# Kernel tuning notes

Measured on AMD Instinct MI355X. Metric: run time of the kernel, lower is better.

Reference implementation:

```python
import jax, jax.numpy as jnp
import numpy as np

B, T = 64, 512
OBS, DM, DS, NL = 115, 128, 8, 3
EMB, NA, H1 = 16, 19, 256


def _ln(x, g, b, eps=1e-5):
    m = jnp.mean(x, -1, keepdims=True)
    v = jnp.mean((x - m) ** 2, -1, keepdims=True)
    return (x - m) * jax.lax.rsqrt(v + eps) * g + b


def _s6(x, h, lng, lnb, w_ig, w_dt, b_dt, a_log, w_b, w_c, d_par, w_out):
    # x: [B,T,DM], h: [B,DM,DS]
    xn = _ln(x, lng, lnb)
    xp = xn @ w_ig.T                               # [B,T,2*DM]
    x_in, z = xp[..., :DM], xp[..., DM:]
    dt = jax.nn.softplus(x_in @ w_dt.T + b_dt)     # [B,T,DM]
    A = -jnp.exp(a_log)                            # [DM,DS]
    bt = x_in @ w_b.T                              # [B,T,DS]
    ct = x_in @ w_c.T                              # [B,T,DS]
    dA = jnp.exp(dt[..., None] * A)                # [B,T,DM,DS]
    upd = (dt * x_in)[..., None] * bt[:, :, None, :]  # [B,T,DM,DS]

    def step(hc, inp):
        dA_t, u_t, c_t = inp
        hn = dA_t * hc + u_t                       # [B,DM,DS]
        y = jnp.einsum('bds,bs->bd', hn, c_t)      # [B,DM]
        return hn, y

    h_f, ys = jax.lax.scan(
        step, h,
        (jnp.swapaxes(dA, 0, 1), jnp.swapaxes(upd, 0, 1), jnp.swapaxes(ct, 0, 1)))
    y = jnp.swapaxes(ys, 0, 1)                     # [B,T,DM]
    ssm = y * jax.nn.silu(z) + x_in * d_par
    return x + ssm @ w_out.T, h_f.reshape(h_f.shape[0], -1)


def _forward(prev_actions, obs, h0, enc_w1, enc_b1, enc_g1, enc_bb1, enc_w2, enc_b2,
             enc_g2, enc_bb2, emb, proj_w, proj_b, proj_g, proj_bb,
             m_ln_g, m_ln_b, m_w_ig, m_w_dt, m_b_dt, m_a_log, m_w_b, m_w_c, m_d, m_w_out,
             fn_g, fn_b, pol_w1, pol_b1, pol_g, pol_bb, pol_w2, pol_b2):
    # MLP encoder: Linear -> LN -> SiLU -> Linear -> LN (final norm)
    e = jax.nn.silu(_ln(obs @ enc_w1.T + enc_b1, enc_g1, enc_bb1))
    e = _ln(e @ enc_w2.T + enc_b2, enc_g2, enc_bb2)
    pa = emb[prev_actions]                         # [B,T,EMB]
    x = jnp.concatenate([e, pa], -1) @ proj_w.T + proj_b
    x = jax.nn.silu(_ln(x, proj_g, proj_bb))
    for i in range(NL):
        x, _ = _s6(x, h0[i].reshape(-1, DM, DS), m_ln_g[i], m_ln_b[i], m_w_ig[i],
                   m_w_dt[i], m_b_dt[i], m_a_log[i], m_w_b[i], m_w_c[i], m_d[i], m_w_out[i])
    x = _ln(x, fn_g, fn_b)
    p = jax.nn.silu(_ln(x @ pol_w1.T + pol_b1, pol_g, pol_bb))
    return p @ pol_w2.T + pol_b2                   # [B,T,NA] policy logits


def setup_inputs() -> dict:
    key = jax.random.key(0)
    ks = iter(jax.random.split(key, 64))
    def n(shape, s=0.05):
        return jax.random.normal(next(ks), shape, dtype=jnp.float32) * s
    return {
        'obs': jax.random.normal(next(ks), (B, T, OBS), dtype=jnp.float32),
        'h0': jnp.zeros((NL, B, DM * DS), jnp.float32),
        'enc_w1': n((H1, OBS)), 'enc_b1': jnp.zeros((H1,)),
        'enc_g1': jnp.ones((H1,)), 'enc_bb1': jnp.zeros((H1,)),
        'enc_w2': n((DM, H1)), 'enc_b2': jnp.zeros((DM,)),
        'enc_g2': jnp.ones((DM,)), 'enc_bb2': jnp.zeros((DM,)),
        'emb': n((NA + 1, EMB), 1.0),
        'proj_w': n((DM, DM + EMB)), 'proj_b': jnp.zeros((DM,)),
        'proj_g': jnp.ones((DM,)), 'proj_bb': jnp.zeros((DM,)),
        'm_ln_g': jnp.ones((NL, DM)), 'm_ln_b': jnp.zeros((NL, DM)),
        'm_w_ig': n((NL, 2 * DM, DM)), 'm_w_dt': n((NL, DM, DM)),
        'm_b_dt': jnp.zeros((NL, DM)),
        'm_a_log': jax.random.uniform(next(ks), (NL, DM, DS), minval=-3.0, maxval=-1.0, dtype=jnp.float32),
        'm_w_b': n((NL, DS, DM)), 'm_w_c': n((NL, DS, DM)),
        'm_d': jnp.ones((NL, DM)), 'm_w_out': n((NL, DM, DM)),
        'fn_g': jnp.ones((DM,)), 'fn_b': jnp.zeros((DM,)),
        'pol_w1': n((DM, DM)), 'pol_b1': jnp.zeros((DM,)),
        'pol_g': jnp.ones((DM,)), 'pol_bb': jnp.zeros((DM,)),
        'pol_w2': n((NA, DM)), 'pol_b2': jnp.zeros((NA,)),
        'prev_actions': jax.random.randint(next(ks), (B, T), 0, NA + 1),
    }


def reference(obs, h0, enc_w1, enc_b1, enc_g1, enc_bb1, enc_w2, enc_b2, enc_g2, enc_bb2,
              emb, proj_w, proj_b, proj_g, proj_bb, m_ln_g, m_ln_b, m_w_ig, m_w_dt,
              m_b_dt, m_a_log, m_w_b, m_w_c, m_d, m_w_out, fn_g, fn_b, pol_w1, pol_b1,
              pol_g, pol_bb, pol_w2, pol_b2, prev_actions):
    return _forward(prev_actions, obs, h0, enc_w1, enc_b1, enc_g1, enc_bb1, enc_w2,
                    enc_b2, enc_g2, enc_bb2, emb, proj_w, proj_b, proj_g, proj_bb,
                    m_ln_g, m_ln_b, m_w_ig, m_w_dt, m_b_dt, m_a_log, m_w_b, m_w_c,
                    m_d, m_w_out, fn_g, fn_b, pol_w1, pol_b1, pol_g, pol_bb, pol_w2, pol_b2)
```

## Files before the change

kernel.cpp:

```cpp
#include <hip/hip_runtime.h>
#include <math.h>

#define BB 64
#define TT 512
#define OBSD 115
#define DMD 128
#define DSD 8
#define NLD 3
#define EMBD 16
#define NAD 19
#define H1D 256
#define NTOK (BB*TT)
#define SSEG 32
#define TSEG (TT/SSEG)

typedef unsigned short ushort_t;
typedef __attribute__((ext_vector_type(8))) short short8;
typedef __attribute__((ext_vector_type(4))) float f32x4;

__device__ __forceinline__ float silu_f(float x){ return x / (1.f + __expf(-x)); }
__device__ __forceinline__ float softplus_f(float x){
  return fmaxf(x, 0.f) + log1pf(__expf(-fabsf(x)));
}
__device__ __forceinline__ ushort_t f2bf(float x){
  unsigned u = __float_as_uint(x);
  unsigned r = (u + 0x7fffu + ((u >> 16) & 1u)) >> 16;
  return (ushort_t)r;
}
__device__ __forceinline__ float b2f(ushort_t x){
  return __uint_as_float(((unsigned)x) << 16);
}
#define MFMA(a,b,c) __builtin_amdgcn_mfma_f32_16x16x32_bf16((a),(b),(c),0,0,0)
#define LOG2E 1.44269504f

struct PJob { const float* src; ushort_t* dst; int N; int K; int Kpad; int rowofs; int Nw; };
struct PJobs { PJob j[20]; };

__global__ __launch_bounds__(256) void k_prep(PJobs P){
  const int job = blockIdx.x >> 2;
  const int sub = blockIdx.x & 3;
  PJob pj = P.j[job];
  const int elems = pj.Nw * pj.Kpad;
  for (int idx = sub*256 + threadIdx.x; idx < elems; idx += 4*256){
    int n = idx / pj.Kpad;
    int k = idx - n*pj.Kpad;
    float v = (n < pj.N && k < pj.K) ? pj.src[(size_t)n*pj.K + k] : 0.f;
    pj.dst[(size_t)(pj.rowofs + n)*pj.Kpad + k] = f2bf(v);
  }
}

__global__ __launch_bounds__(256, 8) void k_enc12p(
    const float* __restrict__ obs, const ushort_t* __restrict__ w1b,
    const float* __restrict__ b1, const float* __restrict__ g1,
    const float* __restrict__ bb1,
    const ushort_t* __restrict__ w2b,
    const float* __restrict__ b2, const float* __restrict__ g2,
    const float* __restrict__ bb2,
    const float* __restrict__ emb, const int* __restrict__ pact,
    const ushort_t* __restrict__ pwb, const float* __restrict__ pb,
    const float* __restrict__ pg, const float* __restrict__ pbb,
    float* __restrict__ X,
    const float* __restrict__ lng, const float* __restrict__ lnb,
    const ushort_t* __restrict__ wigb, const ushort_t* __restrict__ wdbcb,
    const float* __restrict__ bdt,
    ushort_t* __restrict__ XINb, ushort_t* __restrict__ Zb,
    ushort_t* __restrict__ DTb, ushort_t* __restrict__ BTu, ushort_t* __restrict__ CTu,
    const float* __restrict__ alog0,
    float* __restrict__ HLOC, float* __restrict__ PPR)
{
  __shared__ __align__(16) char sm[15104];
  ushort_t* s_obs = (ushort_t*)sm;
  ushort_t* s_e1  = (ushort_t*)sm;
  ushort_t* s_xin = (ushort_t*)sm;
  ushort_t* s_dt  = (ushort_t*)(sm + 4352);
  ushort_t* s_a2  = (ushort_t*)(sm + 8448);
  ushort_t* s_btc = (ushort_t*)(sm + 13824);
  float2*   s_st  = (float2*)(sm + 14080);
  float2*   s_st2 = (float2*)(sm + 14592);

  const int tok0 = blockIdx.x * 16;
  const int bidx = blockIdx.x >> 5;
  const int ch   = blockIdx.x & 31;
  const int tid = threadIdx.x;
  const int lane = tid & 63, w = tid >> 6;
  const int q = lane >> 4, cn = lane & 15;

  {
    const int t = tid >> 4, kc = tid & 15;
    const float* op = obs + (size_t)(tok0 + t)*OBSD;
    short8 v;
    #pragma unroll
    for (int j = 0; j < 8; j++){
      int k = kc*8 + j;
      v[j] = (short)f2bf(k < OBSD ? op[k] : 0.f);
    }
    *(short8*)&s_obs[t*136 + kc*8] = v;
  }
  for (int e = tid; e < 16*32; e += 256){
    int t = e >> 5, k = e & 31;
    float v = 0.f;
    if (k < EMBD){ int a = pact[tok0 + t]; v = emb[(size_t)a*EMBD + k]; }
    s_a2[t*168 + 128 + k] = f2bf(v);
  }
  __syncthreads();

  f32x4 acc[4];
  {
    short8 af[4];
    #pragma unroll
    for (int ks = 0; ks < 4; ks++)
      af[ks] = *(const short8*)&s_obs[cn*136 + ks*32 + q*8];
    #pragma unroll
    for (int nt = 0; nt < 4; nt++){
      const int n0 = (w*4 + nt) * 16;
      f32x4 a = {0.f,0.f,0.f,0.f};
      #pragma unroll
      for (int ks = 0; ks < 4; ks++){
        short8 bf = *(const short8*)&w1b[(size_t)(n0 + cn)*128 + ks*32 + q*8];
        a = MFMA(af[ks], bf, a);
      }
      float bv = b1[n0 + cn];
      #pragma unroll
      for (int r = 0; r < 4; r++) a[r] += bv;
      acc[nt] = a;
    }
    #pragma unroll
    for (int r = 0; r < 4; r++){
      float s = 0.f, s2 = 0.f;
      #pragma unroll
      for (int nt = 0; nt < 4; nt++){ float v = acc[nt][r]; s += v; s2 = fmaf(v, v, s2); }
      s += __shfl_xor(s, 1, 64); s2 += __shfl_xor(s2, 1, 64);
      s += __shfl_xor(s, 2, 64); s2 += __shfl_xor(s2, 2, 64);
      s += __shfl_xor(s, 4, 64); s2 += __shfl_xor(s2, 4, 64);
      s += __shfl_xor(s, 8, 64); s2 += __shfl_xor(s2, 8, 64);
      if (cn == 0) s_st[(q*4 + r)*4 + w] = make_float2(s, s2);
    }
  }
  __syncthreads();

  {
    float mu[4], rs[4];
    #pragma unroll
    for (int r = 0; r < 4; r++){
      const int row = q*4 + r;
      float2 p0 = s_st[row*4+0], p1 = s_st[row*4+1];
      float2 p2 = s_st[row*4+2], p3 = s_st[row*4+3];
      float s = p0.x+p1.x+p2.x+p3.x, s2 = p0.y+p1.y+p2.y+p3.y;
      float m = s * (1.f/256.f);
      mu[r] = m;
      rs[r] = rsqrtf(s2 * (1.f/256.f) - m*m + 1e-5f);
    }
    #pragma unroll
    for (int nt = 0; nt < 4; nt++){
      const int col = (w*4 + nt)*16 + cn;
      float gg = g1[col], bbv = bb1[col];
      #pragma unroll
      for (int r = 0; r < 4; r++){
        float v = (acc[nt][r] - mu[r]) * rs[r] * gg + bbv;
        s_e1[(q*4 + r)*264 + col] = f2bf(silu_f(v));
      }
    }
  }
  __syncthreads();

  f32x4 acc2[2];
  {
    short8 af2[8];
    #pragma unroll
    for (int ks = 0; ks < 8; ks++)
      af2[ks] = *(const short8*)&s_e1[cn*264 + ks*32 + q*8];
    #pragma unroll
    for (int nt = 0; nt < 2; nt++){
      const int n0 = (w*2 + nt) * 16;
      f32x4 a = {0.f,0.f,0.f,0.f};
      #pragma unroll
      for (int ks = 0; ks < 8; ks++){
        short8 bf = *(const short8*)&w2b[(size_t)(n0 + cn)*256 + ks*32 + q*8];
        a = MFMA(af2[ks], bf, a);
      }
      float bv = b2[n0 + cn];
      #pragma unroll
      for (int r = 0; r < 4; r++) a[r] += bv;
      acc2[nt] = a;
    }
    #pragma unroll
    for (int r = 0; r < 4; r++){
      float s = 0.f, s2 = 0.f;
      #pragma unroll
      for (int nt = 0; nt < 2; nt++){ float v = acc2[nt][r]; s += v; s2 = fmaf(v, v, s2); }
      s += __shfl_xor(s, 1, 64); s2 += __shfl_xor(s2, 1, 64);
      s += __shfl_xor(s, 2, 64); s2 += __shfl_xor(s2, 2, 64);
      s += __shfl_xor(s, 4, 64); s2 += __shfl_xor(s2, 4, 64);
      s += __shfl_xor(s, 8, 64); s2 += __shfl_xor(s2, 8, 64);
      if (cn == 0) s_st[(q*4 + r)*4 + w] = make_float2(s, s2);
    }
  }
  __syncthreads();

  {
    float mu[4], rs[4];
    #pragma unroll
    for (int r = 0; r < 4; r++){
      const int row = q*4 + r;
      float2 p0 = s_st[row*4+0], p1 = s_st[row*4+1];
      float2 p2 = s_st[row*4+2], p3 = s_st[row*4+3];
      float s = p0.x+p1.x+p2.x+p3.x, s2 = p0.y+p1.y+p2.y+p3.y;
      float m = s * (1.f/128.f);
      mu[r] = m;
      rs[r] = rsqrtf(s2 * (1.f/128.f) - m*m + 1e-5f);
    }
    #pragma unroll
    for (int nt = 0; nt < 2; nt++){
      const int col = (w*2 + nt)*16 + cn;
      float gg = g2[col], bbv = bb2[col];
      #pragma unroll
      for (int r = 0; r < 4; r++){
        float v = (acc2[nt][r] - mu[r]) * rs[r] * gg + bbv;
        s_a2[(q*4 + r)*168 + col] = f2bf(v);
      }
    }
  }
  __syncthreads();

  f32x4 acc3[2];
  {
    short8 af3[5];
    #pragma unroll
    for (int ks = 0; ks < 5; ks++)
      af3[ks] = *(const short8*)&s_a2[cn*168 + ks*32 + q*8];
    #pragma unroll
    for (int nt = 0; nt < 2; nt++){
      const int n0 = (w*2 + nt) * 16;
      f32x4 a = {0.f,0.f,0.f,0.f};
      #pragma unroll
      for (int ks = 0; ks < 5; ks++){
        short8 bf = *(const short8*)&pwb[(size_t)(n0 + cn)*160 + ks*32 + q*8];
        a = MFMA(af3[ks], bf, a);
      }
      float bv = pb[n0 + cn];
      #pragma unroll
      for (int r = 0; r < 4; r++) a[r] += bv;
      acc3[nt] = a;
    }
    #pragma unroll
    for (int r = 0; r < 4; r++){
      float s = 0.f, s2 = 0.f;
      #pragma unroll
      for (int nt = 0; nt < 2; nt++){ float v = acc3[nt][r]; s += v; s2 = fmaf(v, v, s2); }
      s += __shfl_xor(s, 1, 64); s2 += __shfl_xor(s2, 1, 64);
      s += __shfl_xor(s, 2, 64); s2 += __shfl_xor(s2, 2, 64);
      s += __shfl_xor(s, 4, 64); s2 += __shfl_xor(s2, 4, 64);
      s += __shfl_xor(s, 8, 64); s2 += __shfl_xor(s2, 8, 64);
      if (cn == 0) s_st[(q*4 + r)*4 + w] = make_float2(s, s2);
    }
  }
  __syncthreads();

  {
    float mu[4], rs[4];
    #pragma unroll
    for (int r = 0; r < 4; r++){
      const int row = q*4 + r;
      float2 p0 = s_st[row*4+0], p1 = s_st[row*4+1];
      float2 p2 = s_st[row*4+2], p3 = s_st[row*4+3];
      float s = p0.x+p1.x+p2.x+p3.x, s2 = p0.y+p1.y+p2.y+p3.y;
      float m = s * (1.f/128.f);
      mu[r] = m;
      rs[r] = rsqrtf(s2 * (1.f/128.f) - m*m + 1e-5f);
    }
    float ps[4] = {0.f,0.f,0.f,0.f}, ps2[4] = {0.f,0.f,0.f,0.f};
    #pragma unroll
    for (int nt = 0; nt < 2; nt++){
      const int col = (w*2 + nt)*16 + cn;
      float gg = pg[col], bbv = pbb[col];
      #pragma unroll
      for (int r = 0; r < 4; r++){
        float v = (acc3[nt][r] - mu[r]) * rs[r] * gg + bbv;
        v = silu_f(v);
        acc3[nt][r] = v;
        X[(size_t)(tok0 + q*4 + r)*128 + col] = v;
        ps[r] += v; ps2[r] = fmaf(v, v, ps2[r]);
      }
    }
    #pragma unroll
    for (int r = 0; r < 4; r++){
      float s = ps[r], s2 = ps2[r];
      s += __shfl_xor(s, 1, 64); s2 += __shfl_xor(s2, 1, 64);
      s += __shfl_xor(s, 2, 64); s2 += __shfl_xor(s2, 2, 64);
      s += __shfl_xor(s, 4, 64); s2 += __shfl_xor(s2, 4, 64);
      s += __shfl_xor(s, 8, 64); s2 += __shfl_xor(s2, 8, 64);
      if (cn == 0) s_st2[(q*4 + r)*4 + w] = make_float2(s, s2);
    }
  }
  __syncthreads();

  {
    float mu[4], rs[4];
    #pragma unroll
    for (int r = 0; r < 4; r++){
      const int row = q*4 + r;
      float2 p0 = s_st2[row*4+0], p1 = s_st2[row*4+1];
      float2 p2 = s_st2[row*4+2], p3 = s_st2[row*4+3];
      float s = p0.x+p1.x+p2.x+p3.x, s2 = p0.y+p1.y+p2.y+p3.y;
      float m = s * (1.f/128.f);
      mu[r] = m;
      rs[r] = rsqrtf(s2 * (1.f/128.f) - m*m + 1e-5f);
    }
    #pragma unroll
    for (int nt = 0; nt < 2; nt++){
      const int col = (w*2 + nt)*16 + cn;
      float gg = lng[col], bbv = lnb[col];
      #pragma unroll
      for (int r = 0; r < 4; r++){
        float v = (acc3[nt][r] - mu[r]) * rs[r] * gg + bbv;
        s_a2[(q*4 + r)*168 + col] = f2bf(v);
      }
    }
  }
  __syncthreads();

  {
    short8 af[4];
    #pragma unroll
    for (int ks = 0; ks < 4; ks++)
      af[ks] = *(const short8*)&s_a2[cn*168 + ks*32 + q*8];
    #pragma unroll
    for (int i = 0; i < 4; i++){
      const int n0 = (w*4 + i) * 16;
      f32x4 a = {0.f,0.f,0.f,0.f};
      #pragma unroll
      for (int ks = 0; ks < 4; ks++){
        short8 bf = *(const short8*)&wigb[(size_t)(n0 + cn)*128 + ks*32 + q*8];
        a = MFMA(af[ks], bf, a);
      }
      if (n0 < 128){
        #pragma unroll
        for (int r = 0; r < 4; r++){
          int tr = q*4 + r;
          ushort_t bb = f2bf(a[r]);
          XINb[(size_t)(tok0 + tr)*128 + n0 + cn] = bb;
          s_xin[tr*136 + n0 + cn] = bb;
        }
      } else {
        #pragma unroll
        for (int r = 0; r < 4; r++){
          int tr = q*4 + r;
          Zb[(size_t)(tok0 + tr)*128 + (n0 - 128) + cn] = f2bf(a[r]);
        }
      }
    }
  }
  __syncthreads();

  {
    short8 af2[4];
    #pragma unroll
    for (int ks = 0; ks < 4; ks++)
      af2[ks] = *(const short8*)&s_xin[cn*136 + ks*32 + q*8];
    for (int nt = w; nt < 9; nt += 4){
      const int n0 = nt * 16;
      f32x4 a = {0.f,0.f,0.f,0.f};
      #pragma unroll
      for (int ks = 0; ks < 4; ks++){
        short8 bf = *(const short8*)&wdbcb[(size_t)(n0 + cn)*128 + ks*32 + q*8];
        a = MFMA(af2[ks], bf, a);
      }
      const int col = n0 + cn;
      if (col < 128){
        float bd = bdt[col];
        #pragma unroll
        for (int r = 0; r < 4; r++){
          int tr = q*4 + r;
          ushort_t dv = f2bf(softplus_f(a[r] + bd));
          DTb[(size_t)(tok0 + tr)*128 + col] = dv;
          s_dt[tr*136 + col] = dv;
        }
      } else if (col < 136){
        #pragma unroll
        for (int r = 0; r < 4; r++){
          int tr = q*4 + r;
          ushort_t bb = f2bf(a[r]);
          BTu[(size_t)(tok0 + tr)*8 + (col - 128)] = bb;
          s_btc[tr*8 + (col - 128)] = bb;
        }
      } else {
        #pragma unroll
        for (int r = 0; r < 4; r++)
          CTu[(size_t)(tok0 + q*4 + r)*8 + (col - 136)] = f2bf(a[r]);
      }
    }
  }
  __syncthreads();

  {
    const int d = tid & 127, sh = tid >> 7;
    float A2c[4], hh[4], pp[4];
    #pragma unroll
    for (int j = 0; j < 4; j++){
      A2c[j] = -__expf(alog0[d*8 + sh*4 + j]) * LOG2E;
      hh[j] = 0.f; pp[j] = 1.f;
    }
    #pragma unroll 4
    for (int t = 0; t < 16; t++){
      float dt = b2f(s_dt[t*136 + d]);
      float wv = dt * b2f(s_xin[t*136 + d]);
      #pragma unroll
      for (int j = 0; j < 4; j++){
        float dA = exp2f(dt * A2c[j]);
        hh[j] = fmaf(dA, hh[j], wv * b2f(s_btc[t*8 + sh*4 + j]));
        pp[j] *= dA;
      }
    }
    const size_t o = ((size_t)bidx*SSEG + ch)*1024 + d*8 + sh*4;
    #pragma unroll
    for (int j = 0; j < 4; j++){ HLOC[o+j] = hh[j]; PPR[o+j] = pp[j]; }
  }
}

__global__ __launch_bounds__(256) void k_carry(
    float* __restrict__ HL, const float* __restrict__ PP,
    const float* __restrict__ h0g)
{
  const int idx = blockIdx.x*256 + threadIdx.x;
  const size_t base = (size_t)(idx >> 10) * (SSEG*1024) + (idx & 1023);
  float hl[SSEG], pp[SSEG];
  #pragma unroll
  for (int ch = 0; ch < SSEG; ch++){
    hl[ch] = HL[base + (size_t)ch*1024];
    pp[ch] = PP[base + (size_t)ch*1024];
  }
  float h = h0g[idx];
  #pragma unroll
  for (int ch = 0; ch < SSEG; ch++){
    HL[base + (size_t)ch*1024] = h;
    h = fmaf(pp[ch], h, hl[ch]);
  }
}

#define SMB 17664

__device__ __forceinline__ void phaseB16(
    const ushort_t* DTb, const ushort_t* XINb, const ushort_t* Zb,
    const ushort_t* BTu, const ushort_t* CTu,
    const float* __restrict__ alog, const float* __restrict__ HLpre,
    const float* __restrict__ dpar, const ushort_t* __restrict__ woutb,
    float* __restrict__ X, char* sm, int b, int seg, int tid)
{
  ushort_t* s_dtS = (ushort_t*)sm;
  ushort_t* s_xiS = (ushort_t*)(sm + 4096);
  ushort_t* s_zS  = (ushort_t*)(sm + 8192);
  float*    s_x   = (float*)sm;
  ushort_t* s_a   = (ushort_t*)(sm + 12288);
  ushort_t* s_bt  = (ushort_t*)(sm + 16640);
  ushort_t* s_ct  = (ushort_t*)(sm + 16896);
  float2*   s_st  = (float2*)(sm + 17152);

  const int lane = tid & 63, w = tid >> 6, q = lane >> 4, cn = lane & 15;
  const size_t segtok = (size_t)b*TT + seg*TSEG;

  float xpre[2][4];
  #pragma unroll
  for (int i = 0; i < 2; i++){
    const int n0 = (w*2 + i) * 16;
    #pragma unroll
    for (int r = 0; r < 4; r++)
      xpre[i][r] = X[(segtok + q*4 + r)*128 + n0 + cn];
  }

  ((uint4*)s_dtS)[tid] = ((const uint4*)(DTb  + segtok*128))[tid];
  ((uint4*)s_xiS)[tid] = ((const uint4*)(XINb + segtok*128))[tid];
  ((uint4*)s_zS )[tid] = ((const uint4*)(Zb   + segtok*128))[tid];
  if (tid < 64){
    ((unsigned*)s_bt)[tid] = ((const unsigned*)(BTu + segtok*8))[tid];
    ((unsigned*)s_ct)[tid] = ((const unsigned*)(CTu + segtok*8))[tid];
  }

  const int d2 = (w << 5) | (lane & 31);
  const int sh = lane >> 5;
  float A2h[4], h[4];
  {
    const size_t o = ((size_t)b*SSEG + seg)*1024 + d2*8 + sh*4;
    float4 hv = *(const float4*)(HLpre + o);
    h[0]=hv.x; h[1]=hv.y; h[2]=hv.z; h[3]=hv.w;
    #pragma unroll
    for (int j = 0; j < 4; j++)
      A2h[j] = -__expf(alog[d2*8 + sh*4 + j]) * LOG2E;
  }
  const float dp = dpar[d2];
  __syncthreads();

  #pragma unroll 4
  for (int t = 0; t < 16; t++){
    float dt = b2f(s_dtS[t*128 + d2]);
    float xi = b2f(s_xiS[t*128 + d2]);
    float zv = b2f(s_zS [t*128 + d2]);
    float wv = dt * xi;
    float yp = 0.f;
    #pragma unroll
    for (int j = 0; j < 4; j++){
      float dA = exp2f(dt * A2h[j]);
      h[j] = fmaf(dA, h[j], wv * b2f(s_bt[t*8 + sh*4 + j]));
      yp = fmaf(h[j], b2f(s_ct[t*8 + sh*4 + j]), yp);
    }
    float y = yp + __shfl_xor(yp, 32, 64);
    float ssm = y * silu_f(zv) + xi * dp;
    if (sh == 0) s_a[t*136 + d2] = f2bf(ssm);
  }
  __syncthreads();

  {
    short8 af[4];
    #pragma unroll
    for (int ks = 0; ks < 4; ks++)
      af[ks] = *(const short8*)&s_a[cn*136 + ks*32 + q*8];
    float ps[4] = {0.f,0.f,0.f,0.f}, ps2[4] = {0.f,0.f,0.f,0.f};
    #pragma unroll
    for (int i = 0; i < 2; i++){
      const int n0 = (w*2 + i) * 16;
      short8 bf[4];
      #pragma unroll
      for (int ks = 0; ks < 4; ks++)
        bf[ks] = *(const short8*)&woutb[(size_t)(n0+cn)*128 + ks*32 + q*8];
      f32x4 acc = {0.f,0.f,0.f,0.f};
      #pragma unroll
      for (int ks = 0; ks < 4; ks++) acc = MFMA(af[ks], bf[ks], acc);
      #pragma unroll
      for (int r = 0; r < 4; r++){
        const int tr = q*4 + r;
        const size_t g = (segtok + tr)*128 + n0 + cn;
        float xn = xpre[i][r] + acc[r];
        X[g] = xn;
        s_x[tr*130 + n0 + cn] = xn;
        ps[r] += xn; ps2[r] = fmaf(xn, xn, ps2[r]);
      }
    }
    #pragma unroll
    for (int r = 0; r < 4; r++){
      float s = ps[r], s2 = ps2[r];
      s += __shfl_xor(s, 1, 64); s2 += __shfl_xor(s2, 1, 64);
      s += __shfl_xor(s, 2, 64); s2 += __shfl_xor(s2, 2, 64);
      s += __shfl_xor(s, 4, 64); s2 += __shfl_xor(s2, 4, 64);
      s += __shfl_xor(s, 8, 64); s2 += __shfl_xor(s2, 8, 64);
      if (cn == 0) s_st[(q*4 + r)*4 + w] = make_float2(s, s2);
    }
  }
  __syncthreads();
}

__global__ __launch_bounds__(256, 6) void k_scan2p(
    ushort_t* DTb, ushort_t* XINb, ushort_t* Zb,
    ushort_t* BTu, ushort_t* CTu,
    const float* __restrict__ alog, const float* __restrict__ HLpre,
    const float* __restrict__ dpar, const ushort_t* __restrict__ woutb,
    float* __restrict__ X,
    const float* __restrict__ lng, const float* __restrict__ lnb,
    const ushort_t* __restrict__ wigb, const ushort_t* __restrict__ wdbcb,
    const float* __restrict__ bdt,
    const float* __restrict__ alogn,
    float* __restrict__ HLo, float* __restrict__ PPo)
{
  __shared__ __align__(16) char sm[SMB];
  const int tid = threadIdx.x;
  float*    s_x   = (float*)sm;
  ushort_t* s_xin = (ushort_t*)sm;
  ushort_t* s_dt2 = (ushort_t*)(sm + 4352);
  ushort_t* s_a   = (ushort_t*)(sm + 12288);
  ushort_t* s_btc = (ushort_t*)(sm + 16640);
  float2*   s_st  = (float2*)(sm + 17152);

  const int b = blockIdx.x >> 5;
  const int seg = blockIdx.x & 31;
  const int lane = tid & 63, w = tid >> 6, q = lane >> 4, cn = lane & 15;
  const size_t segtok = (size_t)b*TT + seg*TSEG;

  phaseB16(DTb, XINb, Zb, BTu, CTu, alog, HLpre, dpar, woutb, X, sm, b, seg, tid);

  {
    const int d = tid & 127, half = tid >> 7;
    float g = lng[d], c0v = lnb[d];
    #pragma unroll
    for (int tt = 0; tt < 8; tt++){
      const int t = half*8 + tt;
      float2 p0 = s_st[t*4+0], p1 = s_st[t*4+1];
      float2 p2 = s_st[t*4+2], p3 = s_st[t*4+3];
      float ssum = p0.x+p1.x+p2.x+p3.x, ss2 = p0.y+p1.y+p2.y+p3.y;
      float mu = ssum * (1.f/128.f);
      float rs = rsqrtf(ss2 * (1.f/128.f) - mu*mu + 1e-5f);
      float v = (s_x[t*130 + d] - mu) * rs * g + c0v;
      s_a[t*136 + d] = f2bf(v);
    }
  }
  __syncthreads();

  {
    short8 af[4];
    #pragma unroll
    for (int ks = 0; ks < 4; ks++)
      af[ks] = *(const short8*)&s_a[cn*136 + ks*32 + q*8];
    #pragma unroll
    for (int i = 0; i < 4; i++){
      const int n0 = (w*4 + i) * 16;
      short8 bf[4];
      #pragma unroll
      for (int ks = 0; ks < 4; ks++)
        bf[ks] = *(const short8*)&wigb[(size_t)(n0+cn)*128 + ks*32 + q*8];
      f32x4 acc = {0.f,0.f,0.f,0.f};
      #pragma unroll
      for (int ks = 0; ks < 4; ks++) acc = MFMA(af[ks], bf[ks], acc);
      if (n0 < 128){
        #pragma unroll
        for (int r = 0; r < 4; r++){
          const int tr = q*4 + r;
          ushort_t bb = f2bf(acc[r]);
          XINb[(segtok + tr)*128 + n0 + cn] = bb;
          s_xin[tr*136 + n0 + cn] = bb;
        }
      } else {
        #pragma unroll
        for (int r = 0; r < 4; r++){
          const int tr = q*4 + r;
          Zb[(segtok + tr)*128 + (n0-128) + cn] = f2bf(acc[r]);
        }
      }
    }
  }
  __syncthreads();

  {
    short8 af2[4];
    #pragma unroll
    for (int ks = 0; ks < 4; ks++)
      af2[ks] = *(const short8*)&s_xin[cn*136 + ks*32 + q*8];
    for (int nt = w; nt < 9; nt += 4){
      const int n0 = nt * 16;
      short8 bf[4];
      #pragma unroll
      for (int ks = 0; ks < 4; ks++)
        bf[ks] = *(const short8*)&wdbcb[(size_t)(n0+cn)*128 + ks*32 + q*8];
      f32x4 acc = {0.f,0.f,0.f,0.f};
      #pragma unroll
      for (int ks = 0; ks < 4; ks++) acc = MFMA(af2[ks], bf[ks], acc);
      const int col = n0 + cn;
      if (col < 128){
        float bd = bdt[col];
        #pragma unroll
        for (int r = 0; r < 4; r++){
          const int tr = q*4 + r;
          ushort_t dv = f2bf(softplus_f(acc[r] + bd));
          DTb[(segtok + tr)*128 + col] = dv;
          s_dt2[tr*136 + col] = dv;
        }
      } else if (col < 136){
        #pragma unroll
        for (int r = 0; r < 4; r++){
          const int tr = q*4 + r;
          ushort_t bb = f2bf(acc[r]);
          BTu[(segtok + tr)*8 + (col-128)] = bb;
          s_btc[tr*8 + (col-128)] = bb;
        }
      } else {
        #pragma unroll
        for (int r = 0; r < 4; r++)
          CTu[(segtok + q*4 + r)*8 + (col-136)] = f2bf(acc[r]);
      }
    }
  }
  __syncthreads();

  {
    const int d = tid & 127, sh = tid >> 7;
    float A2n[4], hh[4], pp[4];
    #pragma unroll
    for (int j = 0; j < 4; j++){
      A2n[j] = -__expf(alogn[d*8 + sh*4 + j]) * LOG2E;
      hh[j] = 0.f; pp[j] = 1.f;
    }
    #pragma unroll 4
    for (int t = 0; t < 16; t++){
      float dt = b2f(s_dt2[t*136 + d]);
      float wv = dt * b2f(s_xin[t*136 + d]);
      #pragma unroll
      for (int j = 0; j < 4; j++){
        float dA = exp2f(dt * A2n[j]);
        hh[j] = fmaf(dA, hh[j], wv * b2f(s_btc[t*8 + sh*4 + j]));
        pp[j] *= dA;
      }
    }
    const size_t o = ((size_t)b*SSEG + seg)*1024 + d*8 + sh*4;
    #pragma unroll
    for (int j = 0; j < 4; j++){ HLo[o+j] = hh[j]; PPo[o+j] = pp[j]; }
  }
}

__global__ __launch_bounds__(256, 6) void k_scan2h(
    const ushort_t* DTb, const ushort_t* XINb, const ushort_t* Zb,
    const ushort_t* BTu, const ushort_t* CTu,
    const float* __restrict__ alog, const float* __restrict__ HLpre,
    const float* __restrict__ dpar, const ushort_t* __restrict__ woutb,
    float* __restrict__ X,
    const float* __restrict__ fng, const float* __restrict__ fnb,
    const ushort_t* __restrict__ pw1b, const float* __restrict__ pb1,
    const float* __restrict__ pg, const float* __restrict__ pbb,
    const ushort_t* __restrict__ pw2b, const float* __restrict__ pb2,
    float* __restrict__ out)
{
  __shared__ __align__(16) char sm[SMB];
  const int tid = threadIdx.x;
  float*    s_x  = (float*)sm;
  ushort_t* s_a  = (ushort_t*)(sm + 12288);
  float2*   s_st = (float2*)(sm + 17152);

  const int b = blockIdx.x >> 5;
  const int seg = blockIdx.x & 31;
  const int lane = tid & 63, w = tid >> 6, q = lane >> 4, cn = lane & 15;
  const size_t segtok = (size_t)b*TT + seg*TSEG;

  phaseB16((ushort_t*)DTb, (ushort_t*)XINb, (ushort_t*)Zb,
           (ushort_t*)BTu, (ushort_t*)CTu, alog, HLpre,
           dpar, woutb, X, sm, b, seg, tid);

  {
    const int d = tid & 127, half = tid >> 7;
    float g = fng[d], c0v = fnb[d];
    #pragma unroll
    for (int tt = 0; tt < 8; tt++){
      const int t = half*8 + tt;
      float2 p0 = s_st[t*4+0], p1 = s_st[t*4+1];
      float2 p2 = s_st[t*4+2], p3 = s_st[t*4+3];
      float ssum = p0.x+p1.x+p2.x+p3.x, ss2 = p0.y+p1.y+p2.y+p3.y;
      float mu = ssum * (1.f/128.f);
      float rs = rsqrtf(ss2 * (1.f/128.f) - mu*mu + 1e-5f);
      float v = (s_x[t*130 + d] - mu) * rs * g + c0v;
      s_a[t*136 + d] = f2bf(v);
    }
  }
  __syncthreads();

  {
    short8 af[4];
    #pragma unroll
    for (int ks = 0; ks < 4; ks++)
      af[ks] = *(const short8*)&s_a[cn*136 + ks*32 + q*8];
    float ps[4] = {0.f,0.f,0.f,0.f}, ps2[4] = {0.f,0.f,0.f,0.f};
    #pragma unroll
    for (int i = 0; i < 2; i++){
      const int n0 = (w*2 + i) * 16;
      short8 bf[4];
      #pragma unroll
      for (int ks = 0; ks < 4; ks++)
        bf[ks] = *(const short8*)&pw1b[(size_t)(n0+cn)*128 + ks*32 + q*8];
      float bias = pb1[n0 + cn];
      f32x4 acc = {0.f,0.f,0.f,0.f};
      #pragma unroll
      for (int ks = 0; ks < 4; ks++) acc = MFMA(af[ks], bf[ks], acc);
      #pragma unroll
      for (int r = 0; r < 4; r++){
        float xv = acc[r] + bias;
        s_x[(q*4 + r)*130 + n0 + cn] = xv;
        ps[r] += xv; ps2[r] = fmaf(xv, xv, ps2[r]);
      }
    }
    #pragma unroll
    for (int r = 0; r < 4; r++){
      float s = ps[r], s2 = ps2[r];
      s += __shfl_xor(s, 1, 64); s2 += __shfl_xor(s2, 1, 64);
      s += __shfl_xor(s, 2, 64); s2 += __shfl_xor(s2, 2, 64);
      s += __shfl_xor(s, 4, 64); s2 += __shfl_xor(s2, 4, 64);
      s += __shfl_xor(s, 8, 64); s2 += __shfl_xor(s2, 8, 64);
      if (cn == 0) s_st[(q*4 + r)*4 + w] = make_float2(s, s2);
    }
  }
  __syncthreads();

  {
    const int d = tid & 127, half = tid >> 7;
    float g = pg[d], c0v = pbb[d];
    #pragma unroll
    for (int tt = 0; tt < 8; tt++){
      const int t = half*8 + tt;
      float2 p0 = s_st[t*4+0], p1 = s_st[t*4+1];
      float2 p2 = s_st[t*4+2], p3 = s_st[t*4+3];
      float ssum = p0.x+p1.x+p2.x+p3.x, ss2 = p0.y+p1.y+p2.y+p3.y;
      float mu = ssum * (1.f/128.f);
      float rs = rsqrtf(ss2 * (1.f/128.f) - mu*mu + 1e-5f);
      float v = (s_x[t*130 + d] - mu) * rs * g + c0v;
      s_a[t*136 + d] = f2bf(silu_f(v));
    }
  }
  __syncthreads();

  if (w < 2){
    short8 af[4];
    #pragma unroll
    for (int ks = 0; ks < 4; ks++)
      af[ks] = *(const short8*)&s_a[cn*136 + ks*32 + q*8];
    const int n0 = w * 16;
    short8 bf[4];
    #pragma unroll
    for (int ks = 0; ks < 4; ks++)
      bf[ks] = *(const short8*)&pw2b[(size_t)(n0+cn)*128 + ks*32 + q*8];
    const int col = n0 + cn;
    f32x4 acc = {0.f,0.f,0.f,0.f};
    #pragma unroll
    for (int ks = 0; ks < 4; ks++) acc = MFMA(af[ks], bf[ks], acc);
    if (col < NAD){
      float bias = pb2[col];
      #pragma unroll
      for (int r = 0; r < 4; r++)
        out[(segtok + q*4 + r)*NAD + col] = acc[r] + bias;
    }
  }
}

extern "C" void kernel_launch(void* const* d_in, const int* in_sizes, int n_in,
                              void* d_out, int out_size, void* d_ws, size_t ws_size,
                              hipStream_t stream) {
  const float* obs    = (const float*)d_in[0];
  const float* h0     = (const float*)d_in[1];
  const float* enc_w1 = (const float*)d_in[2];
  const float* enc_b1 = (const float*)d_in[3];
  const float* enc_g1 = (const float*)d_in[4];
  const float* enc_bb1= (const float*)d_in[5];
  const float* enc_w2 = (const float*)d_in[6];
  const float* enc_b2 = (const float*)d_in[7];
  const float* enc_g2 = (const float*)d_in[8];
  const float* enc_bb2= (const float*)d_in[9];
  const float* emb    = (const float*)d_in[10];
  const float* proj_w = (const float*)d_in[11];
  const float* proj_b = (const float*)d_in[12];
  const float* proj_g = (const float*)d_in[13];
  const float* proj_bb= (const float*)d_in[14];
  const float* m_ln_g = (const float*)d_in[15];
  const float* m_ln_b = (const float*)d_in[16];
  const float* m_w_ig = (const float*)d_in[17];
  const float* m_w_dt = (const float*)d_in[18];
  const float* m_b_dt = (const float*)d_in[19];
  const float* m_a_log= (const float*)d_in[20];
  const float* m_w_b  = (const float*)d_in[21];
  const float* m_w_c  = (const float*)d_in[22];
  const float* m_d    = (const float*)d_in[23];
  const float* m_w_out= (const float*)d_in[24];
  const float* fn_g   = (const float*)d_in[25];
  const float* fn_b   = (const float*)d_in[26];
  const float* pol_w1 = (const float*)d_in[27];
  const float* pol_b1 = (const float*)d_in[28];
  const float* pol_g  = (const float*)d_in[29];
  const float* pol_bb = (const float*)d_in[30];
  const float* pol_w2 = (const float*)d_in[31];
  const float* pol_b2 = (const float*)d_in[32];
  const int*   pact   = (const int*)d_in[33];

  float* ws  = (float*)d_ws;
  float* X    = ws;
  float* HLA  = X + (size_t)NTOK*128;
  float* PPA  = HLA + (size_t)BB*SSEG*1024;
  float* HLB  = PPA + (size_t)BB*SSEG*1024;
  float* PPB  = HLB + (size_t)BB*SSEG*1024;
  ushort_t* XINb = (ushort_t*)(PPB + (size_t)BB*SSEG*1024);
  ushort_t* Zb   = XINb + (size_t)NTOK*128;
  ushort_t* DTb  = Zb   + (size_t)NTOK*128;
  ushort_t* BTu  = DTb  + (size_t)NTOK*128;
  ushort_t* CTu  = BTu  + (size_t)NTOK*8;

  ushort_t* W1B   = CTu   + (size_t)NTOK*8;
  ushort_t* W2B   = W1B   + 256*128;
  ushort_t* PWB   = W2B   + 128*256;
  ushort_t* WIGB  = PWB   + 128*160;
  ushort_t* WDBCB = WIGB  + 3*256*128;
  ushort_t* WOUTB = WDBCB + 3*144*128;
  ushort_t* PW1B  = WOUTB + 3*128*128;
  ushort_t* PW2B  = PW1B  + 128*128;

  PJobs P;
  int nj = 0;
  auto add = [&](const float* src, ushort_t* dst, int N, int K, int Kpad, int rowofs, int Nw){
    P.j[nj].src = src; P.j[nj].dst = dst; P.j[nj].N = N; P.j[nj].K = K;
    P.j[nj].Kpad = Kpad; P.j[nj].rowofs = rowofs; P.j[nj].Nw = Nw; nj++;
  };
  add(enc_w1, W1B, 256, 115, 128, 0, 256);
  add(enc_w2, W2B, 128, 256, 256, 0, 128);
  add(proj_w, PWB, 128, 144, 160, 0, 128);
  for (int l = 0; l < NLD; l++)
    add(m_w_ig + (size_t)l*256*128, WIGB + (size_t)l*256*128, 256, 128, 128, 0, 256);
  for (int l = 0; l < NLD; l++){
    add(m_w_dt + (size_t)l*128*128, WDBCB + (size_t)l*144*128, 128, 128, 128, 0,   128);
    add(m_w_b  + (size_t)l*8*128,   WDBCB + (size_t)l*144*128,   8, 128, 128, 128,   8);
    add(m_w_c  + (size_t)l*8*128,   WDBCB + (size_t)l*144*128,   8, 128, 128, 136,   8);
  }
  for (int l = 0; l < NLD; l++)
    add(m_w_out + (size_t)l*128*128, WOUTB + (size_t)l*128*128, 128, 128, 128, 0, 128);
  add(pol_w1, PW1B, 128, 128, 128, 0, 128);
  add(pol_w2, PW2B,  19, 128, 128, 0,  32);

  k_prep<<<20*4, 256, 0, stream>>>(P);
  k_enc12p<<<NTOK/16, 256, 0, stream>>>(obs, W1B, enc_b1, enc_g1, enc_bb1,
      W2B, enc_b2, enc_g2, enc_bb2,
      emb, pact, PWB, proj_b, proj_g, proj_bb, X,
      m_ln_g, m_ln_b, WIGB, WDBCB, m_b_dt,
      XINb, Zb, DTb, BTu, CTu,
      m_a_log, HLA, PPA);

  const int carrygrid = BB*1024/256;
  const int scangrid  = NTOK/16;

  k_carry<<<carrygrid, 256, 0, stream>>>(HLA, PPA, h0);
  k_scan2p<<<scangrid, 256, 0, stream>>>(DTb, XINb, Zb, BTu, CTu,
      m_a_log, HLA, m_d, WOUTB, X,
      m_ln_g + 128, m_ln_b + 128,
      WIGB + (size_t)256*128, WDBCB + (size_t)144*128, m_b_dt + 128,
      m_a_log + 1024, HLB, PPB);
  k_carry<<<carrygrid, 256, 0, stream>>>(HLB, PPB, h0 + (size_t)BB*1024);
  k_scan2p<<<scangrid, 256, 0, stream>>>(DTb, XINb, Zb, BTu, CTu,
      m_a_log + 1024, HLB, m_d + 128, WOUTB + (size_t)128*128, X,
      m_ln_g + 256, m_ln_b + 256,
      WIGB + (size_t)2*256*128, WDBCB + (size_t)2*144*128, m_b_dt + 256,
      m_a_log + 2048, HLA, PPA);
  k_carry<<<carrygrid, 256, 0, stream>>>(HLA, PPA, h0 + (size_t)2*BB*1024);
  k_scan2h<<<scangrid, 256, 0, stream>>>(DTb, XINb, Zb, BTu, CTu,
      m_a_log + 2048, HLA, m_d + 256, WOUTB + (size_t)2*128*128, X,
      fn_g, fn_b, PW1B, pol_b1, pol_g, pol_bb, PW2B, pol_b2,
      (float*)d_out);
}
```

Measured before the change: 402.7 us.

## Parallelize carry scan across four thread groups per state element

The carry kernel used to walk all 32 segments serially in one thread per state element. Now four 64-thread groups each take 8 segments and compute a local composite (product, offset). The composites are exchanged through shared memory, and each group applies its prefix before writing the carry-in values. This raises parallelism and the number of loads in flight for a small latency-bound kernel, at the cost of a block barrier and some extra multiplies.

```diff
diff --git a/kernel.cpp b/kernel.cpp
--- a/kernel.cpp
+++ b/kernel.cpp
@@ -421,19 +421,36 @@
     float* __restrict__ HL, const float* __restrict__ PP,
     const float* __restrict__ h0g)
 {
-  const int idx = blockIdx.x*256 + threadIdx.x;
+  __shared__ float s_P[3*64], s_H[3*64];
+  const int e   = threadIdx.x & 63;
+  const int sub = threadIdx.x >> 6;
+  const int idx = blockIdx.x*64 + e;
   const size_t base = (size_t)(idx >> 10) * (SSEG*1024) + (idx & 1023);
-  float hl[SSEG], pp[SSEG];
+  const int c0 = sub*8;
+
+  float hl[8], pp[8];
   #pragma unroll
-  for (int ch = 0; ch < SSEG; ch++){
-    hl[ch] = HL[base + (size_t)ch*1024];
-    pp[ch] = PP[base + (size_t)ch*1024];
-  }
+  for (int c = 0; c < 8; c++){
+    hl[c] = HL[base + (size_t)(c0+c)*1024];
+    pp[c] = PP[base + (size_t)(c0+c)*1024];
+  }
+  float Pc = 1.f, Hc = 0.f;
+  #pragma unroll
+  for (int c = 0; c < 8; c++){
+    Hc = fmaf(pp[c], Hc, hl[c]);
+    Pc *= pp[c];
+  }
+  if (sub < 3){ s_P[sub*64 + e] = Pc; s_H[sub*64 + e] = Hc; }
   float h = h0g[idx];
+  __syncthreads();
   #pragma unroll
-  for (int ch = 0; ch < SSEG; ch++){
-    HL[base + (size_t)ch*1024] = h;
-    h = fmaf(pp[ch], h, hl[ch]);
+  for (int s = 0; s < 3; s++){
+    if (s < sub) h = fmaf(s_P[s*64 + e], h, s_H[s*64 + e]);
+  }
+  #pragma unroll
+  for (int c = 0; c < 8; c++){
+    HL[base + (size_t)(c0+c)*1024] = h;
+    h = fmaf(pp[c], h, hl[c]);
   }
 }
 
@@ -900,7 +917,7 @@
       XINb, Zb, DTb, BTu, CTu,
       m_a_log, HLA, PPA);
 
-  const int carrygrid = BB*1024/256;
+  const int carrygrid = BB*1024/64;
   const int scangrid  = NTOK/16;
 
   k_carry<<<carrygrid, 256, 0, stream>>>(HLA, PPA, h0);
```

New measurement: 402.0 us. No clear change (-0.2%).
